# Kernel optimization log

Measured on AMD Instinct MI355X. Metric: run time of the kernel, lower is better.

## Reference

```python
import jax, jax.numpy as jnp
import numpy as np

QUERY_DIM = 192
KEY_DIM = 64
DIM_OUT = 128
C = QUERY_DIM + KEY_DIM  # 256
N = 10000
E = 320000
M = 5000


def setup_inputs() -> dict:
    key = jax.random.key(0)
    ks = jax.random.split(key, 16)
    s = 1.0 / np.sqrt(C)
    inp = {
        "query": jax.random.normal(ks[0], (N, QUERY_DIM), jnp.float32),
        "key_idx": jax.random.randint(ks[1], (N,), 0, KEY_DIM),
        "edge_index": jax.random.randint(ks[2], (2, E), 0, N),
        "mask_idx": jnp.sort(jax.random.randint(ks[3], (M,), 0, N)),
        "Wq": jax.random.normal(ks[4], (C, C), jnp.float32) * s,
        "bq": jnp.zeros((C,), jnp.float32),
        "Wk": jax.random.normal(ks[5], (C, C), jnp.float32) * s,
        "bk": jnp.zeros((C,), jnp.float32),
        "Wv": jax.random.normal(ks[6], (C, C), jnp.float32) * s,
        "bv": jnp.zeros((C,), jnp.float32),
        "Ws": jax.random.normal(ks[7], (C, C), jnp.float32) * s,
        "bs": jnp.zeros((C,), jnp.float32),
        "Wo": jax.random.normal(ks[8], (KEY_DIM, DIM_OUT), jnp.float32) * (1.0 / np.sqrt(KEY_DIM)),
        "bo": jnp.zeros((DIM_OUT,), jnp.float32),
    }
    return inp


def reference(query, key_idx, edge_index, mask_idx, Wq, bq, Wk, bk, Wv, bv, Ws, bs, Wo, bo):
    # node features: [N, C] = concat(query, one_hot(key))
    x = jnp.concatenate([query, jax.nn.one_hot(key_idx, KEY_DIM, dtype=query.dtype)], axis=1)
    src, dst = edge_index[0], edge_index[1]  # messages flow src -> dst
    # node-level projections (dense GEMMs), then edge gather
    q_n = x @ Wq + bq
    k_n = x @ Wk + bk
    v_n = x @ Wv + bv
    q = q_n[dst]  # [E, C]
    k = k_n[src]
    v = v_n[src]
    score = jnp.sum(q * k, axis=-1) / jnp.sqrt(jnp.asarray(C, x.dtype))  # [E]
    # per-destination softmax over incoming edges
    m = jax.ops.segment_max(score, dst, num_segments=N)  # [N]
    m = jnp.where(jnp.isfinite(m), m, 0.0)
    e = jnp.exp(score - m[dst])
    denom = jax.ops.segment_sum(e, dst, num_segments=N)
    alpha = e / (denom[dst] + 1e-16)
    # scatter-aggregate weighted values + root/skip connection
    agg = jax.ops.segment_sum(alpha[:, None] * v, dst, num_segments=N)  # [N, C]
    out = agg + (x @ Ws + bs)
    h = jax.nn.relu(out[mask_idx])  # [M, C]
    h = h[:, QUERY_DIM:]  # [M, KEY_DIM]
    return h @ Wo + bo  # [M, DIM_OUT]
```

## Files before the change

kernel.cpp:

```cpp
#include <hip/hip_runtime.h>

#define QDIM 192
#define KDIM 64
#define CDIM 256
#define DOUT 128
#define CAPS 64
#define NVCOL 640
#define NEG_INF __int_as_float(0xFF800000)
#define LDP 200

typedef _Float16 hf2 __attribute__((ext_vector_type(2)));
typedef _Float16 half4 __attribute__((ext_vector_type(4)));
typedef _Float16 half8 __attribute__((ext_vector_type(8)));
typedef float floatx4 __attribute__((ext_vector_type(4)));

#if defined(__has_builtin)
#if __has_builtin(__builtin_amdgcn_fdot2)
#define HAVE_FDOT2 1
#endif
#endif

__device__ __forceinline__ hf2 bc_h2(unsigned u) { return __builtin_bit_cast(hf2, u); }

__device__ __forceinline__ float dot2acc(hf2 a, hf2 b, float c) {
#ifdef HAVE_FDOT2
    return __builtin_amdgcn_fdot2(a, b, c, false);
#else
    return c + (float)a[0] * (float)b[0] + (float)a[1] * (float)b[1];
#endif
}

__global__ __launch_bounds__(256) void prep_kernel(
        const float* __restrict__ query, _Float16* __restrict__ Qh,
        const float* __restrict__ Wq, const float* __restrict__ bq,
        const float* __restrict__ Wk, const float* __restrict__ bk,
        const float* __restrict__ Wv, const float* __restrict__ bv,
        const float* __restrict__ Ws, const float* __restrict__ bs,
        const int* __restrict__ mask, int M,
        _Float16* __restrict__ WhT, float* __restrict__ OB,
        int* __restrict__ deg4, int qchunks, int N) {
    int t = blockIdx.x * blockDim.x + threadIdx.x;
    if (t < qchunks) {
        float4 v = ((const float4*)query)[t];
        half4 h = { (_Float16)v.x, (_Float16)v.y, (_Float16)v.z, (_Float16)v.w };
        ((half4*)Qh)[t] = h;
        return;
    }
    t -= qchunks;
    if (t < NVCOL * QDIM) {
        int v = t / QDIM, r = t - v * QDIM;
        const float* Wseg; int col;
        if (v < 256)      { Wseg = Wq; col = v; }
        else if (v < 512) { Wseg = Wk; col = v - 256; }
        else if (v < 576) { Wseg = Wv; col = QDIM + (v - 512); }
        else              { Wseg = Ws; col = QDIM + (v - 576); }
        WhT[t] = (_Float16)Wseg[(size_t)r * CDIM + col];
        return;
    }
    t -= NVCOL * QDIM;
    if (t < NVCOL * KDIM) {
        int v = t >> 6, kidx = t & 63;
        const float* Wseg; const float* bseg; int col;
        if (v < 256)      { Wseg = Wq; bseg = bq; col = v; }
        else if (v < 512) { Wseg = Wk; bseg = bk; col = v - 256; }
        else if (v < 576) { Wseg = Wv; bseg = bv; col = QDIM + (v - 512); }
        else              { Wseg = Ws; bseg = bs; col = QDIM + (v - 576); }
        OB[t] = Wseg[(size_t)(QDIM + kidx) * CDIM + col] + bseg[col];
        return;
    }
    t -= NVCOL * KDIM;
    if (t < 4 * N) {
        int node = t >> 2;
        int lo = 0, hi = M;
        while (lo < hi) { int mid = (lo + hi) >> 1; if (mask[mid] < node) lo = mid + 1; else hi = mid; }
        bool found = (lo < M) && (mask[lo] == node);
        deg4[t] = found ? 0 : (int)0x80000000;
    }
}

__global__ __launch_bounds__(256) void gemm_nodes(
        const _Float16* __restrict__ Qh, const int* __restrict__ key_idx,
        const _Float16* __restrict__ WhT, const float* __restrict__ OB,
        const int* __restrict__ esrc, const int* __restrict__ edst,
        const int* __restrict__ mask, int M,
        int* deg4, int* __restrict__ adj, int E,
        _Float16* __restrict__ Qbuf, _Float16* __restrict__ Kbuf,
        _Float16* __restrict__ Vbuf, float* __restrict__ Sbuf, int N) {
    __shared__ __align__(16) _Float16 As[64 * LDP];
    __shared__ __align__(16) _Float16 Bs[64 * LDP];
    __shared__ int rowmap[64];
    int tid = threadIdx.x;
    int z = blockIdx.z;
    int bm = blockIdx.x * 64;

    bool doe[2] = {false, false};
    int srcv[2]; int* cnt[2]; size_t abase[2];
    if (z == 0) {
        int stride = gridDim.x * gridDim.y * 256;
        int base = (blockIdx.y * gridDim.x + blockIdx.x) * 256 + tid;
        #pragma unroll
        for (int q = 0; q < 2; q++) {
            int e = base + q * stride;
            if (e < E) {
                int d = edst[e];
                size_t ci = (size_t)d * 4 + (e & 3);
                if (deg4[ci] >= 0) {
                    doe[q] = true; srcv[q] = esrc[e];
                    cnt[q] = &deg4[ci]; abase[q] = ci * CAPS;
                }
            }
        }
        if (bm >= N) {
            #pragma unroll
            for (int q = 0; q < 2; q++)
                if (doe[q]) { int s = atomicAdd(cnt[q], 1); if ((unsigned)s < CAPS) adj[abase[q] + s] = srcv[q]; }
            return;
        }
    } else {
        if (bm >= M) return;
    }

    int bn = (z == 0) ? 256 + blockIdx.y * 64
                      : (blockIdx.y < 4 ? blockIdx.y * 64 : 576);

    if (tid < 64) {
        int rr = bm + tid, g = -1;
        if (z == 0) { if (rr < N) g = rr; }
        else if (rr < M) { int nd = mask[rr]; if (rr == 0 || mask[rr - 1] != nd) g = nd; }
        rowmap[tid] = g;
    }
    __syncthreads();

    #pragma unroll
    for (int it = 0; it < 6; it++) {
        int idx = tid + it * 256;
        int r = idx / 24, q4 = idx % 24;
        int gr = rowmap[r];
        uint4 va = make_uint4(0u, 0u, 0u, 0u);
        if (gr >= 0) va = ((const uint4*)(Qh + (size_t)gr * QDIM))[q4];
        *((uint4*)&As[r * LDP + q4 * 8]) = va;
    }
    #pragma unroll
    for (int it = 0; it < 6; it++) {
        int idx = tid + it * 256;
        int cc = idx / 24, q4 = idx % 24;
        uint4 vb = ((const uint4*)(WhT + (size_t)(bn + cc) * QDIM))[q4];
        *((uint4*)&Bs[cc * LDP + q4 * 8]) = vb;
    }
    __syncthreads();

    int slot[2] = {-1, -1};
    #pragma unroll
    for (int q = 0; q < 2; q++) if (doe[q]) slot[q] = atomicAdd(cnt[q], 1);

    int w = tid >> 6, l = tid & 63;
    int lrow = l & 15, quad = l >> 4;
    floatx4 acc[4] = {{0.f,0.f,0.f,0.f},{0.f,0.f,0.f,0.f},{0.f,0.f,0.f,0.f},{0.f,0.f,0.f,0.f}};

    const _Float16* arow = &As[(w * 16 + lrow) * LDP + quad * 8];
    #pragma unroll
    for (int ks = 0; ks < 6; ks++) {
        half8 af = *(const half8*)(arow + ks * 32);
        #pragma unroll
        for (int nt = 0; nt < 4; nt++) {
            half8 bf = *(const half8*)(&Bs[(nt * 16 + lrow) * LDP + quad * 8 + ks * 32]);
            acc[nt] = __builtin_amdgcn_mfma_f32_16x16x32_f16(af, bf, acc[nt], 0, 0, 0);
        }
    }

    #pragma unroll
    for (int q = 0; q < 2; q++)
        if (doe[q] && (unsigned)slot[q] < CAPS) adj[abase[q] + slot[q]] = srcv[q];

    int ki[4], grs[4];
    #pragma unroll
    for (int reg = 0; reg < 4; reg++) {
        grs[reg] = rowmap[w * 16 + quad * 4 + reg];
        ki[reg] = (grs[reg] >= 0) ? key_idx[grs[reg]] : 0;
    }
    #pragma unroll
    for (int nt = 0; nt < 4; nt++) {
        int gc = bn + nt * 16 + lrow;
        const float* obc = OB + (size_t)gc * KDIM;
        #pragma unroll
        for (int reg = 0; reg < 4; reg++) {
            int gr = grs[reg];
            if (gr >= 0) {
                float v = acc[nt][reg] + obc[ki[reg]];
                if (gc < 256)      Qbuf[(size_t)gr * 256 + gc] = (_Float16)v;
                else if (gc < 512) Kbuf[(size_t)gr * 256 + (gc - 256)] = (_Float16)v;
                else if (gc < 576) Vbuf[(size_t)gr * KDIM + (gc - 512)] = (_Float16)v;
                else               Sbuf[(size_t)gr * KDIM + (gc - 576)] = v;
            }
        }
    }
}

__global__ __launch_bounds__(256) void attend_out(
        const _Float16* __restrict__ Qbuf, const _Float16* __restrict__ Kbuf,
        const _Float16* __restrict__ Vbuf, const float* __restrict__ Sbuf,
        const int* __restrict__ deg4, const int* __restrict__ adj,
        const int* __restrict__ mask, const float* __restrict__ Wo,
        const float* __restrict__ bo, float* __restrict__ out, int M) {
    int w = threadIdx.x >> 6, lane = threadIdx.x & 63;
    int r = blockIdx.x * 4 + w;
    if (r >= M) return;
    int node = mask[r];
    if (r > 0 && mask[r - 1] == node) return;
    int l = lane & 15, g = lane >> 4;

    const uint4* qp = (const uint4*)(Qbuf + (size_t)node * 256 + l * 16);
    uint4 qa = qp[0], qb = qp[1];
    hf2 qh[8] = { bc_h2(qa.x), bc_h2(qa.y), bc_h2(qa.z), bc_h2(qa.w),
                  bc_h2(qb.x), bc_h2(qb.y), bc_h2(qb.z), bc_h2(qb.w) };

    int dn_g = min(deg4[(size_t)node * 4 + g], CAPS);
    int d0 = __shfl(dn_g, 0, 64), d1 = __shfl(dn_g, 16, 64);
    int d2 = __shfl(dn_g, 32, 64), d3 = __shfl(dn_g, 48, 64);
    int O1 = d0, O2 = d0 + d1, O3 = d0 + d1 + d2, T = O3 + d3;
    const size_t base4 = (size_t)node * 4 * CAPS;
    auto fs = [&](int j) -> int {
        int b = (j >= O1) + (j >= O2) + (j >= O3);
        int off = j - (b == 0 ? 0 : b == 1 ? O1 : b == 2 ? O2 : O3);
        return adj[base4 + (size_t)b * CAPS + off];
    };

    float m = NEG_INF, dsum = 0.f;
    float a0 = 0.f, a1 = 0.f, a2 = 0.f, a3 = 0.f;

    uint4 ka, kb; uint2 vv; int s_nxt = 0;
    if (g < T) {
        int s0 = fs(g);
        const uint4* kp = (const uint4*)(Kbuf + (size_t)s0 * 256 + l * 16);
        ka = kp[0]; kb = kp[1];
        vv = *(const uint2*)(Vbuf + (size_t)s0 * KDIM + l * 4);
        s_nxt = (g + 4 < T) ? fs(g + 4) : s0;
    }
    for (int j = g; j < T; j += 4) {
        const uint4* kp2 = (const uint4*)(Kbuf + (size_t)s_nxt * 256 + l * 16);
        uint4 ka2 = kp2[0], kb2 = kp2[1];
        uint2 vv2 = *(const uint2*)(Vbuf + (size_t)s_nxt * KDIM + l * 4);
        int s_aft = (j + 8 < T) ? fs(j + 8) : s_nxt;

        float d = 0.f;
        d = dot2acc(bc_h2(ka.x), qh[0], d);
        d = dot2acc(bc_h2(ka.y), qh[1], d);
        d = dot2acc(bc_h2(ka.z), qh[2], d);
        d = dot2acc(bc_h2(ka.w), qh[3], d);
        d = dot2acc(bc_h2(kb.x), qh[4], d);
        d = dot2acc(bc_h2(kb.y), qh[5], d);
        d = dot2acc(bc_h2(kb.z), qh[6], d);
        d = dot2acc(bc_h2(kb.w), qh[7], d);
        d += __shfl_xor(d, 1, 64);
        d += __shfl_xor(d, 2, 64);
        d += __shfl_xor(d, 4, 64);
        d += __shfl_xor(d, 8, 64);
        float sc = d * 0.0625f;
        float m_new = fmaxf(m, sc);
        float scale = __expf(m - m_new);
        float p = __expf(sc - m_new);
        dsum = dsum * scale + p;
        hf2 v01 = bc_h2(vv.x), v23 = bc_h2(vv.y);
        a0 = a0 * scale + p * (float)v01[0];
        a1 = a1 * scale + p * (float)v01[1];
        a2 = a2 * scale + p * (float)v23[0];
        a3 = a3 * scale + p * (float)v23[1];
        m = m_new;
        ka = ka2; kb = kb2; vv = vv2; s_nxt = s_aft;
    }

    float Mx = fmaxf(m, __shfl_xor(m, 16, 64));
    Mx = fmaxf(Mx, __shfl_xor(Mx, 32, 64));
    float wgt = (m == NEG_INF) ? 0.f : __expf(m - Mx);
    float ds = dsum * wgt;
    ds += __shfl_xor(ds, 16, 64);
    ds += __shfl_xor(ds, 32, 64);
    a0 *= wgt; a1 *= wgt; a2 *= wgt; a3 *= wgt;
    a0 += __shfl_xor(a0, 16, 64); a0 += __shfl_xor(a0, 32, 64);
    a1 += __shfl_xor(a1, 16, 64); a1 += __shfl_xor(a1, 32, 64);
    a2 += __shfl_xor(a2, 16, 64); a2 += __shfl_xor(a2, 32, 64);
    a3 += __shfl_xor(a3, 16, 64); a3 += __shfl_xor(a3, 32, 64);
    float inv = 1.f / (ds + 1e-16f);

    float4 s4 = *((const float4*)(Sbuf + (size_t)node * KDIM + l * 4));
    float h0 = fmaxf(a0 * inv + s4.x, 0.f);
    float h1 = fmaxf(a1 * inv + s4.y, 0.f);
    float h2 = fmaxf(a2 * inv + s4.z, 0.f);
    float h3 = fmaxf(a3 * inv + s4.w, 0.f);

    float o0 = bo[lane], o1 = bo[lane + 64];
    #pragma unroll
    for (int c = 0; c < KDIM; c++) {
        float hc = (c & 3) == 0 ? h0 : (c & 3) == 1 ? h1 : (c & 3) == 2 ? h2 : h3;
        float hv = __shfl(hc, c >> 2, 64);
        o0 += hv * Wo[c * DOUT + lane];
        o1 += hv * Wo[c * DOUT + 64 + lane];
    }
    int rr = r;
    do {
        out[(size_t)rr * DOUT + lane] = o0;
        out[(size_t)rr * DOUT + 64 + lane] = o1;
        rr++;
    } while (rr < M && mask[rr] == node);
}

extern "C" void kernel_launch(void* const* d_in, const int* in_sizes, int n_in,
                              void* d_out, int out_size, void* d_ws, size_t ws_size,
                              hipStream_t stream) {
    const float* query    = (const float*)d_in[0];
    const int* key_idx    = (const int*)d_in[1];
    const int* edge_index = (const int*)d_in[2];
    const int* mask_idx   = (const int*)d_in[3];
    const float* Wq = (const float*)d_in[4];
    const float* bq = (const float*)d_in[5];
    const float* Wk = (const float*)d_in[6];
    const float* bk = (const float*)d_in[7];
    const float* Wv = (const float*)d_in[8];
    const float* bv = (const float*)d_in[9];
    const float* Ws = (const float*)d_in[10];
    const float* bs = (const float*)d_in[11];
    const float* Wo = (const float*)d_in[12];
    const float* bo = (const float*)d_in[13];

    int N = in_sizes[0] / QDIM;
    int E = in_sizes[2] / 2;
    int M = in_sizes[3];
    const int* esrc = edge_index;
    const int* edst = edge_index + E;

    char* wsb = (char*)d_ws;
    size_t off = 0;
    auto alloc = [&](size_t nbytes) { char* p = wsb + off; off += (nbytes + 15) & ~15ull; return p; };
    _Float16* Qh   = (_Float16*)alloc((size_t)N * QDIM * 2);
    _Float16* WhT  = (_Float16*)alloc((size_t)NVCOL * QDIM * 2);
    float* OB      = (float*)alloc((size_t)NVCOL * KDIM * 4);
    _Float16* Qbuf = (_Float16*)alloc((size_t)N * 256 * 2);
    _Float16* Kbuf = (_Float16*)alloc((size_t)N * 256 * 2);
    _Float16* Vbuf = (_Float16*)alloc((size_t)N * KDIM * 2);
    float* Sbuf    = (float*)alloc((size_t)N * KDIM * 4);
    int*   deg4    = (int*)alloc((size_t)N * 4 * 4);
    int*   adj     = (int*)alloc((size_t)N * 4 * CAPS * 4);

    int qchunks = N * QDIM / 4;
    int total1 = qchunks + NVCOL * QDIM + NVCOL * KDIM + 4 * N;
    prep_kernel<<<(total1 + 255) / 256, 256, 0, stream>>>(
        query, Qh, Wq, bq, Wk, bk, Wv, bv, Ws, bs, mask_idx, M, WhT, OB, deg4, qchunks, N);

    int xa = (N + 63) / 64, xm = (M + 63) / 64;
    dim3 ggrid((unsigned)max(xa, xm), 5, 2);
    gemm_nodes<<<ggrid, 256, 0, stream>>>(Qh, key_idx, WhT, OB, esrc, edst,
                                          mask_idx, M, deg4, adj, E,
                                          Qbuf, Kbuf, Vbuf, Sbuf, N);

    attend_out<<<(M + 3) / 4, 256, 0, stream>>>(Qbuf, Kbuf, Vbuf, Sbuf, deg4, adj,
                                                mask_idx, Wo, bo, (float*)d_out, M);
}
```

Measured before the change: 134.9 us.

## Load GEMM fragments directly from global memory instead of staging through LDS

The node GEMM kernel no longer stages A and B tiles in shared memory. Each wave now loads its MFMA A fragments into registers and streams B fragments straight from global memory, which removes both __syncthreads and the roughly 51 KB of LDS per block that limited occupancy. Out-of-range and duplicate mask rows are clamped rather than masked, so they redundantly write identical values. The adjacency atomics move to the end of the kernel. In exchange, the B tile is fetched by every wave from cache instead of being shared once through LDS.

```diff
diff --git a/kernel.cpp b/kernel.cpp
--- a/kernel.cpp
+++ b/kernel.cpp
@@ -7,7 +7,6 @@
 #define CAPS 64
 #define NVCOL 640
 #define NEG_INF __int_as_float(0xFF800000)
-#define LDP 200
 
 typedef _Float16 hf2 __attribute__((ext_vector_type(2)));
 typedef _Float16 half4 __attribute__((ext_vector_type(4)));
@@ -86,15 +85,12 @@
         int* deg4, int* __restrict__ adj, int E,
         _Float16* __restrict__ Qbuf, _Float16* __restrict__ Kbuf,
         _Float16* __restrict__ Vbuf, float* __restrict__ Sbuf, int N) {
-    __shared__ __align__(16) _Float16 As[64 * LDP];
-    __shared__ __align__(16) _Float16 Bs[64 * LDP];
-    __shared__ int rowmap[64];
     int tid = threadIdx.x;
     int z = blockIdx.z;
     int bm = blockIdx.x * 64;
 
     bool doe[2] = {false, false};
-    int srcv[2]; int* cnt[2]; size_t abase[2];
+    int srcv[2]; size_t ci[2] = {0, 0};
     if (z == 0) {
         int stride = gridDim.x * gridDim.y * 256;
         int base = (blockIdx.y * gridDim.x + blockIdx.x) * 256 + tid;
@@ -103,17 +99,16 @@
             int e = base + q * stride;
             if (e < E) {
                 int d = edst[e];
-                size_t ci = (size_t)d * 4 + (e & 3);
-                if (deg4[ci] >= 0) {
-                    doe[q] = true; srcv[q] = esrc[e];
-                    cnt[q] = &deg4[ci]; abase[q] = ci * CAPS;
+                size_t c = (size_t)d * 4 + (e & 3);
+                if (deg4[c] >= 0) {
+                    doe[q] = true; srcv[q] = esrc[e]; ci[q] = c;
                 }
             }
         }
         if (bm >= N) {
             #pragma unroll
             for (int q = 0; q < 2; q++)
-                if (doe[q]) { int s = atomicAdd(cnt[q], 1); if ((unsigned)s < CAPS) adj[abase[q] + s] = srcv[q]; }
+                if (doe[q]) { int s = atomicAdd(&deg4[ci[q]], 1); if ((unsigned)s < CAPS) adj[ci[q] * CAPS + s] = srcv[q]; }
             return;
         }
     } else {
@@ -123,60 +118,33 @@
     int bn = (z == 0) ? 256 + blockIdx.y * 64
                       : (blockIdx.y < 4 ? blockIdx.y * 64 : 576);
 
-    if (tid < 64) {
-        int rr = bm + tid, g = -1;
-        if (z == 0) { if (rr < N) g = rr; }
-        else if (rr < M) { int nd = mask[rr]; if (rr == 0 || mask[rr - 1] != nd) g = nd; }
-        rowmap[tid] = g;
-    }
-    __syncthreads();
-
-    #pragma unroll
-    for (int it = 0; it < 6; it++) {
-        int idx = tid + it * 256;
-        int r = idx / 24, q4 = idx % 24;
-        int gr = rowmap[r];
-        uint4 va = make_uint4(0u, 0u, 0u, 0u);
-        if (gr >= 0) va = ((const uint4*)(Qh + (size_t)gr * QDIM))[q4];
-        *((uint4*)&As[r * LDP + q4 * 8]) = va;
-    }
-    #pragma unroll
-    for (int it = 0; it < 6; it++) {
-        int idx = tid + it * 256;
-        int cc = idx / 24, q4 = idx % 24;
-        uint4 vb = ((const uint4*)(WhT + (size_t)(bn + cc) * QDIM))[q4];
-        *((uint4*)&Bs[cc * LDP + q4 * 8]) = vb;
-    }
-    __syncthreads();
-
-    int slot[2] = {-1, -1};
-    #pragma unroll
-    for (int q = 0; q < 2; q++) if (doe[q]) slot[q] = atomicAdd(cnt[q], 1);
-
     int w = tid >> 6, l = tid & 63;
     int lrow = l & 15, quad = l >> 4;
+
+    int ra = w * 16 + lrow;
+    int gra = (z == 0) ? min(bm + ra, N - 1) : mask[min(bm + ra, M - 1)];
+    const _Float16* abase = Qh + (size_t)gra * QDIM + quad * 8;
+    half8 af[6];
+    #pragma unroll
+    for (int ks = 0; ks < 6; ks++) af[ks] = *(const half8*)(abase + ks * 32);
+
     floatx4 acc[4] = {{0.f,0.f,0.f,0.f},{0.f,0.f,0.f,0.f},{0.f,0.f,0.f,0.f},{0.f,0.f,0.f,0.f}};
-
-    const _Float16* arow = &As[(w * 16 + lrow) * LDP + quad * 8];
-    #pragma unroll
-    for (int ks = 0; ks < 6; ks++) {
-        half8 af = *(const half8*)(arow + ks * 32);
+    #pragma unroll
+    for (int nt = 0; nt < 4; nt++) {
+        const _Float16* bbase = WhT + (size_t)(bn + nt * 16 + lrow) * QDIM + quad * 8;
         #pragma unroll
-        for (int nt = 0; nt < 4; nt++) {
-            half8 bf = *(const half8*)(&Bs[(nt * 16 + lrow) * LDP + quad * 8 + ks * 32]);
-            acc[nt] = __builtin_amdgcn_mfma_f32_16x16x32_f16(af, bf, acc[nt], 0, 0, 0);
+        for (int ks = 0; ks < 6; ks++) {
+            half8 bf = *(const half8*)(bbase + ks * 32);
+            acc[nt] = __builtin_amdgcn_mfma_f32_16x16x32_f16(af[ks], bf, acc[nt], 0, 0, 0);
         }
     }
 
-    #pragma unroll
-    for (int q = 0; q < 2; q++)
-        if (doe[q] && (unsigned)slot[q] < CAPS) adj[abase[q] + slot[q]] = srcv[q];
-
     int ki[4], grs[4];
     #pragma unroll
     for (int reg = 0; reg < 4; reg++) {
-        grs[reg] = rowmap[w * 16 + quad * 4 + reg];
-        ki[reg] = (grs[reg] >= 0) ? key_idx[grs[reg]] : 0;
+        int re = w * 16 + quad * 4 + reg;
+        grs[reg] = (z == 0) ? min(bm + re, N - 1) : mask[min(bm + re, M - 1)];
+        ki[reg] = key_idx[grs[reg]];
     }
     #pragma unroll
     for (int nt = 0; nt < 4; nt++) {
@@ -185,15 +153,17 @@
         #pragma unroll
         for (int reg = 0; reg < 4; reg++) {
             int gr = grs[reg];
-            if (gr >= 0) {
-                float v = acc[nt][reg] + obc[ki[reg]];
-                if (gc < 256)      Qbuf[(size_t)gr * 256 + gc] = (_Float16)v;
-                else if (gc < 512) Kbuf[(size_t)gr * 256 + (gc - 256)] = (_Float16)v;
-                else if (gc < 576) Vbuf[(size_t)gr * KDIM + (gc - 512)] = (_Float16)v;
-                else               Sbuf[(size_t)gr * KDIM + (gc - 576)] = v;
-            }
+            float v = acc[nt][reg] + obc[ki[reg]];
+            if (gc < 256)      Qbuf[(size_t)gr * 256 + gc] = (_Float16)v;
+            else if (gc < 512) Kbuf[(size_t)gr * 256 + (gc - 256)] = (_Float16)v;
+            else if (gc < 576) Vbuf[(size_t)gr * KDIM + (gc - 512)] = (_Float16)v;
+            else               Sbuf[(size_t)gr * KDIM + (gc - 576)] = v;
         }
     }
+
+    #pragma unroll
+    for (int q = 0; q < 2; q++)
+        if (doe[q]) { int s = atomicAdd(&deg4[ci[q]], 1); if ((unsigned)s < CAPS) adj[ci[q] * CAPS + s] = srcv[q]; }
 }
 
 __global__ __launch_bounds__(256) void attend_out(
```

Result: slower. 138.6 us (+2.7%).
